# Kernel optimization log

Measured on AMD Instinct MI355X. Metric: run time of the kernel, lower is better.

## Reference

```python
import jax, jax.numpy as jnp
import numpy as np

DIM = 3072
HEADS = 24
HD = 128  # head_dim
RANK = 64
COND = 1024      # (512//8)*(512//8)*16//64
BLOCK = 2048     # main latent tokens
SEQ = BLOCK + COND
NIP = 64         # image_emb tokens
LORA_W = 1.0     # lora_weights[0]
ALPHA_SCALE = 1.0  # network_alpha / rank = 64/64
IP_SCALE = 1.0


def setup_inputs() -> dict:
    key = jax.random.key(0)
    ks = jax.random.split(key, 21)
    d = {}
    d["hidden_states"] = jax.random.normal(ks[0], (1, SEQ, DIM), jnp.float32)
    d["image_emb"] = jax.random.normal(ks[1], (1, NIP, DIM), jnp.float32)
    d["rope_cos"] = jax.random.uniform(ks[2], (SEQ, HD), jnp.float32)
    d["rope_sin"] = jax.random.uniform(ks[3], (SEQ, HD), jnp.float32)
    d["wq"] = jax.random.normal(ks[4], (DIM, DIM), jnp.float32) * 0.02
    d["bq"] = jax.random.normal(ks[5], (DIM,), jnp.float32) * 0.02
    d["wk"] = jax.random.normal(ks[6], (DIM, DIM), jnp.float32) * 0.02
    d["bk"] = jax.random.normal(ks[7], (DIM,), jnp.float32) * 0.02
    d["wv"] = jax.random.normal(ks[8], (DIM, DIM), jnp.float32) * 0.02
    d["bv"] = jax.random.normal(ks[9], (DIM,), jnp.float32) * 0.02
    d["norm_q_w"] = jax.random.uniform(ks[10], (HD,), jnp.float32, 0.5, 1.5)
    d["norm_k_w"] = jax.random.uniform(ks[11], (HD,), jnp.float32, 0.5, 1.5)
    d["q_down"] = jax.random.normal(ks[12], (RANK, DIM), jnp.float32) / RANK
    d["q_up"] = jax.random.normal(ks[13], (DIM, RANK), jnp.float32) * 0.02
    d["k_down"] = jax.random.normal(ks[14], (RANK, DIM), jnp.float32) / RANK
    d["k_up"] = jax.random.normal(ks[15], (DIM, RANK), jnp.float32) * 0.02
    d["v_down"] = jax.random.normal(ks[16], (RANK, DIM), jnp.float32) / RANK
    d["v_up"] = jax.random.normal(ks[17], (DIM, RANK), jnp.float32) * 0.02
    d["wk_ip"] = jax.random.normal(ks[18], (DIM, DIM), jnp.float32) * 0.02
    d["wv_ip"] = jax.random.normal(ks[19], (DIM, DIM), jnp.float32) * 0.02
    return d


def _rmsnorm(x, w, eps):
    v = jnp.mean(jnp.square(x), axis=-1, keepdims=True)
    y = x * jax.lax.rsqrt(v + eps)
    return y if w is None else y * w


def _heads(x, b):  # (B,S,DIM) -> (B,H,S,HD)
    return x.reshape(b, -1, HEADS, HD).transpose(0, 2, 1, 3)


def _rope(x, cos, sin):
    # diffusers apply_rotary_emb, use_real, unbind_dim=-1
    x1 = x[..., 0::2]
    x2 = x[..., 1::2]
    rot = jnp.stack([-x2, x1], axis=-1).reshape(x.shape)
    return x * cos[None, None] + rot * sin[None, None]


def _sdpa(q, k, v, bias=None):
    s = jnp.einsum("bhqd,bhkd->bhqk", q, k) / jnp.sqrt(jnp.float32(q.shape[-1]))
    if bias is not None:
        s = s + bias
    p = jax.nn.softmax(s, axis=-1)
    return jnp.einsum("bhqk,bhkd->bhqd", p, v)


def reference(hidden_states, image_emb, rope_cos, rope_sin,
              wq, bq, wk, bk, wv, bv, norm_q_w, norm_k_w,
              q_down, q_up, k_down, k_up, v_down, v_up, wk_ip, wv_ip):
    B = hidden_states.shape[0]

    # base QKV projections
    q = hidden_states @ wq.T + bq
    k = hidden_states @ wk.T + bk
    v = hidden_states @ wv.T + bv

    # original (pre-LoRA, pre-norm, pre-RoPE) query on the main block for IP attention
    original_query = _heads(hidden_states[:, :BLOCK] @ wq.T + bq, B)

    # masked LoRA add (n_loras=1): only tokens [BLOCK, BLOCK+COND) contribute
    pos = jnp.arange(SEQ)
    tok_mask = ((pos >= BLOCK) & (pos < BLOCK + COND)).astype(hidden_states.dtype)
    hm = hidden_states * tok_mask[None, :, None]
    q = q + LORA_W * ALPHA_SCALE * ((hm @ q_down.T) @ q_up.T)
    k = k + LORA_W * ALPHA_SCALE * ((hm @ k_down.T) @ k_up.T)
    v = v + LORA_W * ALPHA_SCALE * ((hm @ v_down.T) @ v_up.T)

    q = _heads(q, B)
    k = _heads(k, B)
    v = _heads(v, B)

    # per-head RMSNorm (attn.norm_q / attn.norm_k, eps=1e-6 in Flux)
    q = _rmsnorm(q, norm_q_w, 1e-6)
    k = _rmsnorm(k, norm_k_w, 1e-6)

    # IP-adapter cross attention with the original query
    ip_k = _rmsnorm(_heads(image_emb @ wk_ip.T, B), None, 1e-5)
    ip_v = _heads(image_emb @ wv_ip.T, B)
    ip_out = _sdpa(original_query, ip_k, ip_v)  # (B,H,BLOCK,HD)
    ip_out = ip_out.transpose(0, 2, 1, 3).reshape(B, -1, DIM)

    # RoPE on q/k
    q = _rope(q, rope_cos, rope_sin)
    k = _rope(k, rope_cos, rope_sin)

    # attention bias: main-block queries see everything; cond queries only their own block
    m = jnp.ones((SEQ, SEQ), jnp.float32)
    m = m.at[:BLOCK, :].set(0.0)
    m = m.at[BLOCK:BLOCK + COND, BLOCK:BLOCK + COND].set(0.0)
    bias = (m * -1e20)[None, None]

    out = _sdpa(q, k, v, bias)  # (B,H,SEQ,HD)
    out = out.transpose(0, 2, 1, 3).reshape(B, SEQ, DIM)

    main = out[:, :BLOCK, :] + IP_SCALE * ip_out
    return main
```

## Files before the change

### kernel.cpp

```cpp
#include <hip/hip_runtime.h>
#include <stdint.h>

#define DIM 3072
#define HEADS 24
#define HD 128
#define RANKN 64
#define CONDN 1024
#define BLK 2048
#define SEQN 3072
#define NIPN 64

typedef __attribute__((ext_vector_type(8))) short s8v;
typedef __attribute__((ext_vector_type(4))) float fx4;

static __device__ __forceinline__ unsigned short f2bf(float f){
  union{float f; unsigned u;} v; v.f=f;
  unsigned r = v.u + 0x7FFFu + ((v.u>>16)&1u);
  return (unsigned short)(r>>16);
}

#define GL16(g,l) __builtin_amdgcn_global_load_lds((const __attribute__((address_space(1))) void*)(g), (__attribute__((address_space(3))) void*)(l), 16, 0, 0)
#define MFMA(a,b,c) __builtin_amdgcn_mfma_f32_16x16x32_bf16((a),(b),(c),0,0,0)

__global__ __launch_bounds__(256) void cvt_f32_bf16(const float* __restrict__ src,
                                                    unsigned short* __restrict__ dst, int n4){
  int i = blockIdx.x*256 + threadIdx.x;
  if (i < n4){
    float4 v = ((const float4*)src)[i];
    ushort4 o;
    o.x = f2bf(v.x); o.y = f2bf(v.y); o.z = f2bf(v.z); o.w = f2bf(v.w);
    ((ushort4*)dst)[i] = o;
  }
}

__global__ __launch_bounds__(256) void lora_down_g(const unsigned short* __restrict__ A,
                                                   const unsigned short* __restrict__ D0,
                                                   const unsigned short* __restrict__ D1,
                                                   unsigned short* __restrict__ outb){
  __shared__ unsigned short As[128*64];
  __shared__ unsigned short Bs[64*64];
  int tid = threadIdx.x, lane = tid & 63, w = tid >> 6;
  int l15 = lane & 15, l16 = lane >> 4;
  int z = blockIdx.z;
  int m0 = blockIdx.y * 128;
  const unsigned short* Dw = z ? D1 : D0;
  int wr = w * 32;
  fx4 acc[2][4] = {};
  for (int kt = 0; kt < DIM; kt += 64){
    #pragma unroll
    for (int i = 0; i < 4; i++){
      int p = i*256 + tid;
      int row = p >> 3, cc = p & 7;
      int gc = cc ^ (row & 7);
      GL16(A + (size_t)(m0+row)*DIM + kt + gc*8, As + p*8);
    }
    #pragma unroll
    for (int i = 0; i < 2; i++){
      int p = i*256 + tid;
      int row = p >> 3, cc = p & 7;
      int gc = cc ^ (row & 7);
      GL16(Dw + (size_t)row*DIM + kt + gc*8, Bs + p*8);
    }
    __syncthreads();
    #pragma unroll
    for (int kk = 0; kk < 2; kk++){
      s8v af[2], bfr[4];
      #pragma unroll
      for (int t = 0; t < 2; t++){
        int rowa = wr + t*16 + l15;
        int ca = (kk*4 + l16) ^ (rowa & 7);
        af[t] = *(const s8v*)(As + rowa*64 + ca*8);
      }
      #pragma unroll
      for (int t = 0; t < 4; t++){
        int rowb = t*16 + l15;
        int cb = (kk*4 + l16) ^ (rowb & 7);
        bfr[t] = *(const s8v*)(Bs + rowb*64 + cb*8);
      }
      #pragma unroll
      for (int mt = 0; mt < 2; mt++)
        #pragma unroll
        for (int nt = 0; nt < 4; nt++)
          acc[mt][nt] = MFMA(af[mt], bfr[nt], acc[mt][nt]);
    }
    __syncthreads();
  }
  #pragma unroll
  for (int mt = 0; mt < 2; mt++)
    #pragma unroll
    for (int j = 0; j < 4; j++){
      int row = m0 + wr + mt*16 + l16*4 + j;
      #pragma unroll
      for (int nt = 0; nt < 4; nt++){
        int col = nt*16 + l15;
        outb[((size_t)z*CONDN + row)*64 + col] = f2bf(acc[mt][nt][j]);
      }
    }
}

#define BM 128
#define BN 128
#define BK 64
__global__ __launch_bounds__(256) void gemm_qkv2(
    const unsigned short* __restrict__ hs_bf,
    const unsigned short* __restrict__ ie_bf,
    const unsigned short* __restrict__ Wq,
    const unsigned short* __restrict__ Wk,
    const unsigned short* __restrict__ Wv,
    const unsigned short* __restrict__ Wik,
    const unsigned short* __restrict__ Wiv,
    const float* __restrict__ bq, const float* __restrict__ bk, const float* __restrict__ bv,
    const unsigned short* __restrict__ downb,
    const unsigned short* __restrict__ upk,
    const unsigned short* __restrict__ upv,
    float* __restrict__ qb, float* __restrict__ kb, float* __restrict__ vb,
    float* __restrict__ ipk_pre, float* __restrict__ ipv_pre)
{
  __shared__ unsigned short As[BM*BK];
  __shared__ unsigned short Bs[BN*BK];
  int tid = threadIdx.x, lane = tid & 63, w = tid >> 6;
  int l15 = lane & 15, l16 = lane >> 4;
  int x = blockIdx.x, y = blockIdx.y;
  int z = x / 24, n = x % 24;
  bool is_main = true;
  int z2 = 0;
  if (z == 0 && y >= 16){
    int sub = (y - 16)*24 + n;
    if (sub >= 48) return;
    is_main = false; z2 = sub / 24; n = sub % 24;
  }
  int m0 = y * 128;
  const unsigned short* A = is_main ? hs_bf : ie_bf;
  const unsigned short* B = is_main ? (z==0 ? Wq : (z==1 ? Wk : Wv))
                                    : (z2 ? Wiv : Wik);
  int n0 = n * 128;
  int wr = (w >> 1) * 64, wc = (w & 1) * 64;

  fx4 acc[4][4] = {};

  for (int kt = 0; kt < DIM; kt += BK){
    #pragma unroll
    for (int i = 0; i < 4; i++){
      int p = i*256 + tid;
      int row = p >> 3, cc = p & 7;
      int gc = cc ^ (row & 7);
      int arow = is_main ? (m0 + row) : (row > 63 ? 63 : row);
      GL16(A + (size_t)arow*DIM + kt + gc*8, As + p*8);
      GL16(B + (size_t)(n0+row)*DIM + kt + gc*8, Bs + p*8);
    }
    __syncthreads();
    #pragma unroll
    for (int kk = 0; kk < 2; kk++){
      s8v af[4], bfr[4];
      #pragma unroll
      for (int t = 0; t < 4; t++){
        int rowa = wr + t*16 + l15;
        int ca = (kk*4 + l16) ^ (rowa & 7);
        af[t] = *(const s8v*)(As + rowa*BK + ca*8);
        int rowb = wc + t*16 + l15;
        int cb = (kk*4 + l16) ^ (rowb & 7);
        bfr[t] = *(const s8v*)(Bs + rowb*BK + cb*8);
      }
      #pragma unroll
      for (int mt = 0; mt < 4; mt++)
        #pragma unroll
        for (int nt = 0; nt < 4; nt++)
          acc[mt][nt] = MFMA(af[mt], bfr[nt], acc[mt][nt]);
    }
    __syncthreads();
  }

  if (!is_main){
    float* outp = z2 ? ipv_pre : ipk_pre;
    #pragma unroll
    for (int mt = 0; mt < 4; mt++)
      #pragma unroll
      for (int j = 0; j < 4; j++){
        int row = wr + mt*16 + l16*4 + j;
        if (row < 64){
          #pragma unroll
          for (int nt = 0; nt < 4; nt++)
            outp[(size_t)row*DIM + n0 + wc + nt*16 + l15] = acc[mt][nt][j];
        }
      }
    return;
  }

  if (z >= 1 && m0 >= BLK){
    const unsigned short* dwn = downb + (size_t)(z-1)*CONDN*64 + (size_t)(m0-BLK)*64;
    const unsigned short* up  = (z==1) ? upk : upv;
    #pragma unroll
    for (int i = 0; i < 4; i++){
      int p = i*256 + tid;
      int row = p >> 3, cc = p & 7;
      int gc = cc ^ (row & 7);
      GL16(dwn + (size_t)row*64 + gc*8, As + p*8);
      GL16(up + (size_t)(n0+row)*64 + gc*8, Bs + p*8);
    }
    __syncthreads();
    #pragma unroll
    for (int kk = 0; kk < 2; kk++){
      s8v af[4], bfr[4];
      #pragma unroll
      for (int t = 0; t < 4; t++){
        int rowa = wr + t*16 + l15;
        int ca = (kk*4 + l16) ^ (rowa & 7);
        af[t] = *(const s8v*)(As + rowa*64 + ca*8);
        int rowb = wc + t*16 + l15;
        int cb = (kk*4 + l16) ^ (rowb & 7);
        bfr[t] = *(const s8v*)(Bs + rowb*64 + cb*8);
      }
      #pragma unroll
      for (int mt = 0; mt < 4; mt++)
        #pragma unroll
        for (int nt = 0; nt < 4; nt++)
          acc[mt][nt] = MFMA(af[mt], bfr[nt], acc[mt][nt]);
    }
  }

  {
    const float* bias = z==0 ? bq : (z==1 ? bk : bv);
    float* C = z==0 ? qb : (z==1 ? kb : vb);
    float bv4[4];
    #pragma unroll
    for (int nt = 0; nt < 4; nt++) bv4[nt] = bias[n0 + wc + nt*16 + l15];
    #pragma unroll
    for (int mt = 0; mt < 4; mt++)
      #pragma unroll
      for (int j = 0; j < 4; j++){
        int row = m0 + wr + mt*16 + l16*4 + j;
        float* crow = C + (size_t)row*DIM;
        #pragma unroll
        for (int nt = 0; nt < 4; nt++){
          int col = n0 + wc + nt*16 + l15;
          crow[col] = acc[mt][nt][j] + bv4[nt];
        }
      }
  }
}

__global__ __launch_bounds__(256) void norm_rope(const float* __restrict__ src,
                                                 unsigned short* __restrict__ dst,
                                                 const float* __restrict__ wt,
                                                 const float* __restrict__ rc,
                                                 const float* __restrict__ rs,
                                                 int S, float qscale){
  int tid = threadIdx.x, lane = tid & 63, w = tid >> 6;
  int r = blockIdx.x*4 + w;
  int pos = r % S, h = r / S;
  const float* x = src + (size_t)pos*DIM + h*HD;
  float2 xv = *(const float2*)(x + 2*lane);
  float ss = xv.x*xv.x + xv.y*xv.y;
  #pragma unroll
  for (int o = 1; o < 64; o <<= 1) ss += __shfl_xor(ss, o);
  float rr = rsqrtf(ss*(1.f/128.f) + 1e-6f);
  float y0 = xv.x*rr*wt[2*lane], y1 = xv.y*rr*wt[2*lane+1];
  float2 cv = *(const float2*)(rc + (size_t)pos*HD + 2*lane);
  float2 sv = *(const float2*)(rs + (size_t)pos*HD + 2*lane);
  float o0 = (y0*cv.x - y1*sv.x)*qscale;
  float o1 = (y1*cv.y + y0*sv.y)*qscale;
  ushort2 ov; ov.x = f2bf(o0); ov.y = f2bf(o1);
  *(ushort2*)(dst + ((size_t)h*S + pos)*HD + 2*lane) = ov;
}

__global__ __launch_bounds__(256) void ipk_norm_bf(const float* __restrict__ src,
                                                   unsigned short* __restrict__ dst){
  int tid = threadIdx.x, lane = tid & 63, w = tid >> 6;
  int r = blockIdx.x*4 + w;
  int pos = r / HEADS, h = r % HEADS;
  const float* x = src + (size_t)pos*DIM + h*HD;
  float2 xv = *(const float2*)(x + 2*lane);
  float ss = xv.x*xv.x + xv.y*xv.y;
  #pragma unroll
  for (int o = 1; o < 64; o <<= 1) ss += __shfl_xor(ss, o);
  float rr = rsqrtf(ss*(1.f/128.f) + 1e-5f);
  ushort2 ov; ov.x = f2bf(xv.x*rr); ov.y = f2bf(xv.y*rr);
  *(ushort2*)(dst + ((size_t)h*NIPN + pos)*HD + 2*lane) = ov;
}

__global__ __launch_bounds__(256) void ipv_transpose(const float* __restrict__ ipv,
                                                     unsigned short* __restrict__ vt){
  int h = blockIdx.x, tid = threadIdx.x;
  #pragma unroll
  for (int i = 0; i < 32; i++){
    int idx = i*256 + tid;
    int d = idx >> 6, key = idx & 63;
    vt[((size_t)h*HD + d)*64 + key] = f2bf(ipv[(size_t)key*DIM + h*HD + d]);
  }
}

__global__ __launch_bounds__(256) void v_transpose(const float* __restrict__ v,
                                                   unsigned short* __restrict__ Vt){
  __shared__ float t[64][129];
  int h = blockIdx.y, p0 = blockIdx.x*64, tid = threadIdx.x;
  int dcol = tid & 127, prow2 = tid >> 7;
  #pragma unroll
  for (int i = 0; i < 32; i++){
    int pos = i*2 + prow2;
    t[pos][dcol] = v[(size_t)(p0+pos)*DIM + h*HD + dcol];
  }
  __syncthreads();
  int pos = tid & 63, dbase = tid >> 6;
  #pragma unroll
  for (int i = 0; i < 32; i++){
    int d = i*4 + dbase;
    Vt[((size_t)h*HD + d)*SEQN + p0 + pos] = f2bf(t[pos][d]);
  }
}

__global__ __launch_bounds__(256) void ip_attn_m(const float* __restrict__ qb,
                                                 const unsigned short* __restrict__ ipk_bf,
                                                 const unsigned short* __restrict__ ipv_t,
                                                 float* __restrict__ out){
  __shared__ unsigned short Ks[64*HD];
  __shared__ unsigned short Vs[HD*64];
  __shared__ unsigned short Ps[4][16*64];
  int tid = threadIdx.x, lane = tid & 63, w = tid >> 6;
  int l15 = lane & 15, l16 = lane >> 4;
  int h = blockIdx.y;
  int q0 = blockIdx.x*64 + w*16;
  const unsigned short* Kh = ipk_bf + (size_t)h*NIPN*HD;
  const unsigned short* Vh = ipv_t + (size_t)h*HD*NIPN;

  #pragma unroll
  for (int i = 0; i < 4; i++){
    int p = i*256 + tid;
    int row = p >> 4, cc = p & 15;
    int gc = cc ^ (row & 7);
    GL16(Kh + (size_t)row*HD + gc*8, Ks + p*8);
  }
  #pragma unroll
  for (int i = 0; i < 4; i++){
    int p = i*256 + tid;
    int row = p >> 3, cc = p & 7;
    int gc = cc ^ (row & 7);
    GL16(Vh + (size_t)row*64 + gc*8, Vs + p*8);
  }

  s8v qf[4];
  #pragma unroll
  for (int kf = 0; kf < 4; kf++){
    const float* qp = qb + (size_t)(q0 + l15)*DIM + h*HD + kf*32 + l16*8;
    float4 a = *(const float4*)qp;
    float4 b = *(const float4*)(qp + 4);
    s8v f;
    f[0]=(short)f2bf(a.x); f[1]=(short)f2bf(a.y); f[2]=(short)f2bf(a.z); f[3]=(short)f2bf(a.w);
    f[4]=(short)f2bf(b.x); f[5]=(short)f2bf(b.y); f[6]=(short)f2bf(b.z); f[7]=(short)f2bf(b.w);
    qf[kf] = f;
  }
  __syncthreads();

  fx4 s[4] = {};
  #pragma unroll
  for (int ct = 0; ct < 4; ct++){
    #pragma unroll
    for (int kk = 0; kk < 4; kk++){
      int row = ct*16 + l15;
      int c = (kk*4 + l16) ^ (row & 7);
      s8v b = *(const s8v*)(Ks + row*HD + c*8);
      s[ct] = MFMA(qf[kk], b, s[ct]);
    }
  }
  const float SC = 0.08838834764831845f;
  float lrow[4];
  #pragma unroll
  for (int j = 0; j < 4; j++){
    #pragma unroll
    for (int ct = 0; ct < 4; ct++) s[ct][j] *= SC;
    float v = fmaxf(fmaxf(s[0][j], s[1][j]), fmaxf(s[2][j], s[3][j]));
    #pragma unroll
    for (int o2 = 1; o2 < 16; o2 <<= 1) v = fmaxf(v, __shfl_xor(v, o2));
    float sum = 0.f;
    #pragma unroll
    for (int ct = 0; ct < 4; ct++){
      float p = __expf(s[ct][j] - v);
      s[ct][j] = p;
      sum += p;
    }
    #pragma unroll
    for (int o2 = 1; o2 < 16; o2 <<= 1) sum += __shfl_xor(sum, o2);
    lrow[j] = sum;
  }

  #pragma unroll
  for (int ct = 0; ct < 4; ct++)
    #pragma unroll
    for (int j = 0; j < 4; j++){
      int row = l16*4 + j;
      int cidx = ct*16 + l15;
      Ps[w][row*64 + (((cidx>>3) ^ (row&7))<<3) + (cidx&7)] = f2bf(s[ct][j]);
    }
  asm volatile("s_waitcnt lgkmcnt(0)" ::: "memory");
  s8v pa[2];
  #pragma unroll
  for (int kk = 0; kk < 2; kk++){
    int c = (kk*4 + l16) ^ (l15 & 7);
    pa[kk] = *(const s8v*)(&Ps[w][l15*64 + c*8]);
  }
  fx4 o[8] = {};
  #pragma unroll
  for (int nt = 0; nt < 8; nt++){
    #pragma unroll
    for (int kk = 0; kk < 2; kk++){
      int row = nt*16 + l15;
      int c = (kk*4 + l16) ^ (row & 7);
      s8v bv = *(const s8v*)(Vs + row*64 + c*8);
      o[nt] = MFMA(pa[kk], bv, o[nt]);
    }
  }
  #pragma unroll
  for (int nt = 0; nt < 8; nt++)
    #pragma unroll
    for (int j = 0; j < 4; j++){
      int row = q0 + l16*4 + j;
      int d = nt*16 + l15;
      out[(size_t)row*DIM + h*HD + d] = o[nt][j] / lrow[j];
    }
}

#define QB 128
#define KVB 64
#define PSTR 72
__global__ __launch_bounds__(512, 4) void flash_attn_split(const unsigned short* __restrict__ Qn,
                                                           const unsigned short* __restrict__ Kn,
                                                           const unsigned short* __restrict__ Vt,
                                                           float* __restrict__ po0,
                                                           float* __restrict__ po1,
                                                           float* __restrict__ pm,
                                                           float* __restrict__ pl){
  __shared__ unsigned short Ks[KVB*HD];
  __shared__ unsigned short Vs[HD*KVB];
  __shared__ unsigned short Ps[8][16*PSTR];
  int tid = threadIdx.x, lane = tid & 63, w = tid >> 6;
  int l15 = lane & 15, l16 = lane >> 4;
  int b = blockIdx.x;
  int swz = (b & 7) * 96 + (b >> 3);
  int sp = swz / 384;
  int rem = swz - sp*384;
  int h = rem >> 4;
  int qt = rem & 15;
  int q0 = qt*QB + w*16;
  const unsigned short* Qh = Qn + (size_t)h*BLK*HD;
  const unsigned short* Kh = Kn + (size_t)h*SEQN*HD;
  const unsigned short* Vh = Vt + (size_t)h*HD*SEQN;
  const int kvbase = sp * (SEQN/2);
  const int NT = (SEQN/2) / KVB;

  s8v qf[4];
  #pragma unroll
  for (int kf = 0; kf < 4; kf++)
    qf[kf] = *(const s8v*)(Qh + (size_t)(q0 + l15)*HD + kf*32 + l16*8);

  fx4 o[8] = {};
  float mrow[4], lrow[4];
  #pragma unroll
  for (int j = 0; j < 4; j++){ mrow[j] = -1e30f; lrow[j] = 0.f; }

  for (int t = 0; t < NT; t++){
    int kv0 = kvbase + t*KVB;
    #pragma unroll
    for (int i = 0; i < 2; i++){
      int p = i*512 + tid;
      int row = p >> 4, cc = p & 15;
      int gc = cc ^ (row & 7);
      GL16(Kh + (size_t)(kv0+row)*HD + gc*8, Ks + p*8);
    }
    #pragma unroll
    for (int i = 0; i < 2; i++){
      int p = i*512 + tid;
      int row = p >> 3, cc = p & 7;
      int gc = cc ^ (row & 7);
      GL16(Vh + (size_t)row*SEQN + kv0 + gc*8, Vs + p*8);
    }
    __syncthreads();

    fx4 s[4] = {};
    #pragma unroll
    for (int ct = 0; ct < 4; ct++){
      #pragma unroll
      for (int kk = 0; kk < 4; kk++){
        int row = ct*16 + l15;
        int c = (kk*4 + l16) ^ (row & 7);
        s8v bb = *(const s8v*)(Ks + row*HD + c*8);
        s[ct] = MFMA(qf[kk], bb, s[ct]);
      }
    }
    float pmax[4], rssum[4];
    #pragma unroll
    for (int j = 0; j < 4; j++){
      float v = fmaxf(fmaxf(s[0][j], s[1][j]), fmaxf(s[2][j], s[3][j]));
      #pragma unroll
      for (int o2 = 1; o2 < 16; o2 <<= 1) v = fmaxf(v, __shfl_xor(v, o2));
      pmax[j] = v;
      rssum[j] = 0.f;
    }
    float need = 0.f;
    #pragma unroll
    for (int j = 0; j < 4; j++) need = fmaxf(need, pmax[j] - mrow[j]);
    if (__any(need > 8.f)){
      float alpha[4];
      #pragma unroll
      for (int j = 0; j < 4; j++){
        float mnew = fmaxf(mrow[j], pmax[j]);
        alpha[j] = __expf(mrow[j] - mnew);
        mrow[j] = mnew;
      }
      #pragma unroll
      for (int nt = 0; nt < 8; nt++)
        #pragma unroll
        for (int j = 0; j < 4; j++) o[nt][j] *= alpha[j];
      #pragma unroll
      for (int j = 0; j < 4; j++) lrow[j] *= alpha[j];
    }
    #pragma unroll
    for (int ct = 0; ct < 4; ct++)
      #pragma unroll
      for (int j = 0; j < 4; j++){
        float p = __expf(s[ct][j] - mrow[j]);
        s[ct][j] = p;
        rssum[j] += p;
      }
    #pragma unroll
    for (int j = 0; j < 4; j++){
      #pragma unroll
      for (int o2 = 1; o2 < 16; o2 <<= 1) rssum[j] += __shfl_xor(rssum[j], o2);
      lrow[j] += rssum[j];
    }

    #pragma unroll
    for (int ct = 0; ct < 4; ct++)
      #pragma unroll
      for (int j = 0; j < 4; j++){
        int row = l16*4 + j;
        int cidx = ct*16 + l15;
        Ps[w][row*PSTR + cidx] = f2bf(s[ct][j]);
      }
    asm volatile("s_waitcnt lgkmcnt(0)" ::: "memory");
    s8v pa[2];
    #pragma unroll
    for (int kk = 0; kk < 2; kk++)
      pa[kk] = *(const s8v*)(&Ps[w][l15*PSTR + (kk*4 + l16)*8]);
    #pragma unroll
    for (int nt = 0; nt < 8; nt++){
      #pragma unroll
      for (int kk = 0; kk < 2; kk++){
        int row = nt*16 + l15;
        int c = (kk*4 + l16) ^ (row & 7);
        s8v bvv = *(const s8v*)(Vs + row*KVB + c*8);
        o[nt] = MFMA(pa[kk], bvv, o[nt]);
      }
    }
    __syncthreads();
  }

  float* pop = sp ? po1 : po0;
  #pragma unroll
  for (int nt = 0; nt < 8; nt++)
    #pragma unroll
    for (int j = 0; j < 4; j++){
      int row = q0 + l16*4 + j;
      int d = nt*16 + l15;
      pop[((size_t)h*BLK + row)*HD + d] = o[nt][j];
    }
  if (l15 == 0){
    #pragma unroll
    for (int j = 0; j < 4; j++){
      int row = q0 + l16*4 + j;
      pm[(size_t)sp*HEADS*BLK + h*BLK + row] = mrow[j];
      pl[(size_t)sp*HEADS*BLK + h*BLK + row] = lrow[j];
    }
  }
}

__global__ __launch_bounds__(256) void flash_merge(const float* __restrict__ po0,
                                                   const float* __restrict__ po1,
                                                   const float* __restrict__ pm,
                                                   const float* __restrict__ pl,
                                                   float* __restrict__ out){
  int tid = threadIdx.x, lane = tid & 63, w = tid >> 6;
  int r = blockIdx.x*4 + w;
  int h = r >> 11, pos = r & 2047;
  float m0 = pm[r], m1 = pm[HEADS*BLK + r];
  float l0 = pl[r], l1 = pl[HEADS*BLK + r];
  float mx = fmaxf(m0, m1);
  float a0 = __expf(m0 - mx), a1 = __expf(m1 - mx);
  float li = 1.f / (l0*a0 + l1*a1);
  float s0 = a0*li, s1 = a1*li;
  size_t base = ((size_t)h*BLK + pos)*HD + 2*lane;
  float2 x0 = *(const float2*)(po0 + base);
  float2 x1 = *(const float2*)(po1 + base);
  float* op = out + (size_t)pos*DIM + h*HD + 2*lane;
  float2 cv = *(const float2*)op;
  cv.x += x0.x*s0 + x1.x*s1;
  cv.y += x0.y*s0 + x1.y*s1;
  *(float2*)op = cv;
}

extern "C" void kernel_launch(void* const* d_in, const int* in_sizes, int n_in,
                              void* d_out, int out_size, void* d_ws, size_t ws_size,
                              hipStream_t stream){
  (void)in_sizes; (void)n_in; (void)out_size;
  const float* hs       = (const float*)d_in[0];
  const float* image_emb= (const float*)d_in[1];
  const float* rope_cos = (const float*)d_in[2];
  const float* rope_sin = (const float*)d_in[3];
  const float* wq = (const float*)d_in[4];
  const float* bq = (const float*)d_in[5];
  const float* wk = (const float*)d_in[6];
  const float* bk = (const float*)d_in[7];
  const float* wv = (const float*)d_in[8];
  const float* bv = (const float*)d_in[9];
  const float* norm_q_w = (const float*)d_in[10];
  const float* norm_k_w = (const float*)d_in[11];
  const float* k_down = (const float*)d_in[14];
  const float* k_up   = (const float*)d_in[15];
  const float* v_down = (const float*)d_in[16];
  const float* v_up   = (const float*)d_in[17];
  const float* wk_ip  = (const float*)d_in[18];
  const float* wv_ip  = (const float*)d_in[19];
  float* out = (float*)d_out;

  char* ws = (char*)d_ws;
  size_t off = 0;
  auto alloc = [&](size_t bytes){ void* p = ws + off; off += (bytes + 255) & ~(size_t)255; return p; };
  unsigned short* hs_bf = (unsigned short*)alloc((size_t)SEQN*DIM*2);
  unsigned short* ie_bf = (unsigned short*)alloc((size_t)NIPN*DIM*2);
  unsigned short* w_bf[5];
  for (int i = 0; i < 5; i++) w_bf[i] = (unsigned short*)alloc((size_t)DIM*DIM*2);
  unsigned short* lw_bf[4];
  for (int i = 0; i < 4; i++) lw_bf[i] = (unsigned short*)alloc((size_t)RANKN*DIM*2);
  unsigned short* downb = (unsigned short*)alloc((size_t)2*CONDN*RANKN*2);
  float* qb = (float*)alloc((size_t)BLK*DIM*4);
  float* kb = (float*)alloc((size_t)SEQN*DIM*4);
  float* vb = (float*)alloc((size_t)SEQN*DIM*4);
  float* ipk_pre = (float*)alloc((size_t)NIPN*DIM*4);
  float* ipv_pre = (float*)alloc((size_t)NIPN*DIM*4);
  unsigned short* ipk_bf = (unsigned short*)alloc((size_t)HEADS*NIPN*HD*2);
  unsigned short* ipv_t  = (unsigned short*)alloc((size_t)HEADS*HD*NIPN*2);
  float* pm  = (float*)alloc((size_t)2*HEADS*BLK*4);
  float* pl  = (float*)alloc((size_t)2*HEADS*BLK*4);
  if (off > ws_size) return;

  unsigned short* Qn = w_bf[0];
  unsigned short* Kn = w_bf[1];
  unsigned short* Vt = w_bf[2];
  float* po0 = qb;
  float* po1 = kb;

  int n4;
  n4 = SEQN*DIM/4;
  cvt_f32_bf16<<<(n4+255)/256, 256, 0, stream>>>(hs, hs_bf, n4);
  n4 = NIPN*DIM/4;
  cvt_f32_bf16<<<(n4+255)/256, 256, 0, stream>>>(image_emb, ie_bf, n4);

  n4 = DIM*DIM/4;
  cvt_f32_bf16<<<(n4+255)/256, 256, 0, stream>>>(wq, w_bf[0], n4);
  cvt_f32_bf16<<<(n4+255)/256, 256, 0, stream>>>(wk, w_bf[1], n4);
  cvt_f32_bf16<<<(n4+255)/256, 256, 0, stream>>>(wv, w_bf[2], n4);
  cvt_f32_bf16<<<(n4+255)/256, 256, 0, stream>>>(wk_ip, w_bf[3], n4);
  cvt_f32_bf16<<<(n4+255)/256, 256, 0, stream>>>(wv_ip, w_bf[4], n4);

  n4 = RANKN*DIM/4;
  cvt_f32_bf16<<<(n4+255)/256, 256, 0, stream>>>(k_down, lw_bf[0], n4);
  cvt_f32_bf16<<<(n4+255)/256, 256, 0, stream>>>(v_down, lw_bf[1], n4);
  cvt_f32_bf16<<<(n4+255)/256, 256, 0, stream>>>(k_up,   lw_bf[2], n4);
  cvt_f32_bf16<<<(n4+255)/256, 256, 0, stream>>>(v_up,   lw_bf[3], n4);

  lora_down_g<<<dim3(1, CONDN/128, 2), 256, 0, stream>>>(hs_bf + (size_t)BLK*DIM,
      lw_bf[0], lw_bf[1], downb);

  gemm_qkv2<<<dim3(72, 24), 256, 0, stream>>>(hs_bf, ie_bf,
      w_bf[0], w_bf[1], w_bf[2], w_bf[3], w_bf[4],
      bq, bk, bv, downb, lw_bf[2], lw_bf[3],
      qb, kb, vb, ipk_pre, ipv_pre);

  ipk_norm_bf<<<(NIPN*HEADS)/4, 256, 0, stream>>>(ipk_pre, ipk_bf);
  ipv_transpose<<<HEADS, 256, 0, stream>>>(ipv_pre, ipv_t);

  const float SC = 0.08838834764831845f;
  norm_rope<<<(BLK*HEADS)/4, 256, 0, stream>>>(qb, Qn, norm_q_w, rope_cos, rope_sin, BLK, SC);
  norm_rope<<<(SEQN*HEADS)/4, 256, 0, stream>>>(kb, Kn, norm_k_w, rope_cos, rope_sin, SEQN, 1.0f);
  v_transpose<<<dim3(SEQN/64, HEADS), 256, 0, stream>>>(vb, Vt);

  ip_attn_m<<<dim3(BLK/64, HEADS), 256, 0, stream>>>(qb, ipk_bf, ipv_t, out);
  flash_attn_split<<<768, 512, 0, stream>>>(Qn, Kn, Vt, po0, po1, pm, pl);
  flash_merge<<<(HEADS*BLK)/4, 256, 0, stream>>>(po0, po1, pm, pl, out);
}
```

Baseline: 616.5 us.

## Rewrite QKV GEMM with 256x256 tiles, double-buffered LDS and XCD-aware block mapping

Replaces the 128x128 single-buffered QKV/IP projection GEMM with a 512-thread kernel that computes 256x256 output tiles. The K loop now double-buffers LDS, splitting the next-tile loads into quarter chunks that are interleaved with MFMA phases under s_setprio. A flattened 408-block grid is remapped so that consecutive tiles land on the same XCD. The goal is to raise arithmetic intensity and hide global-load latency. The cost is higher register and LDS pressure, and 408 large tiles may leave the last wave unevenly spread across CUs.

```diff
diff --git a/kernel.cpp b/kernel.cpp
--- a/kernel.cpp
+++ b/kernel.cpp
@@ -98,10 +98,7 @@
     }
 }
 
-#define BM 128
-#define BN 128
-#define BK 64
-__global__ __launch_bounds__(256) void gemm_qkv2(
+__global__ __launch_bounds__(512, 2) void gemm_256(
     const unsigned short* __restrict__ hs_bf,
     const unsigned short* __restrict__ ie_bf,
     const unsigned short* __restrict__ Wq,
@@ -116,125 +113,194 @@
     float* __restrict__ qb, float* __restrict__ kb, float* __restrict__ vb,
     float* __restrict__ ipk_pre, float* __restrict__ ipv_pre)
 {
-  __shared__ unsigned short As[BM*BK];
-  __shared__ unsigned short Bs[BN*BK];
+  __shared__ unsigned short Ab[2][16384];
+  __shared__ unsigned short Bb[2][16384];
   int tid = threadIdx.x, lane = tid & 63, w = tid >> 6;
+  int wm = w >> 2, wn = w & 3;
   int l15 = lane & 15, l16 = lane >> 4;
-  int x = blockIdx.x, y = blockIdx.y;
-  int z = x / 24, n = x % 24;
-  bool is_main = true;
-  int z2 = 0;
-  if (z == 0 && y >= 16){
-    int sub = (y - 16)*24 + n;
-    if (sub >= 48) return;
-    is_main = false; z2 = sub / 24; n = sub % 24;
-  }
-  int m0 = y * 128;
-  const unsigned short* A = is_main ? hs_bf : ie_bf;
-  const unsigned short* B = is_main ? (z==0 ? Wq : (z==1 ? Wk : Wv))
-                                    : (z2 ? Wiv : Wik);
-  int n0 = n * 128;
-  int wr = (w >> 1) * 64, wc = (w & 1) * 64;
-
-  fx4 acc[4][4] = {};
-
-  for (int kt = 0; kt < DIM; kt += BK){
+
+  int b = blockIdx.x;
+  int id = (b & 7) * 51 + (b >> 3);
+  int z, mt, ntile;
+  if (id < 96){ z = 0; mt = id / 12; ntile = id % 12; }
+  else if (id < 240){ z = 1; int r = id - 96; mt = r / 12; ntile = r % 12; }
+  else if (id < 384){ z = 2; int r = id - 240; mt = r / 12; ntile = r % 12; }
+  else { z = 3; int r = id - 384; mt = r / 12; ntile = r % 12; }
+  const bool is_ip = (z == 3);
+  int z2 = is_ip ? mt : 0;
+  int m0 = is_ip ? 0 : mt * 256;
+  int n0 = ntile * 256;
+  const unsigned short* A = is_ip ? ie_bf : hs_bf;
+  const unsigned short* B = is_ip ? (z2 ? Wiv : Wik)
+                                  : (z == 0 ? Wq : (z == 1 ? Wk : Wv));
+
+  fx4 acc[8][4] = {};
+  s8v af[8], bfr[8];
+
+  auto stA = [&](int buf, int half, int kt){
+    #pragma unroll
+    for (int i = 0; i < 2; i++){
+      int p = i*512 + tid;
+      int row = p >> 3, cc = p & 7, gc = cc ^ (row & 7);
+      int ar = m0 + half*128 + row;
+      if (is_ip && ar > 63) ar = 63;
+      GL16(A + (size_t)ar*DIM + kt + gc*8, &Ab[buf][half*8192 + p*8]);
+    }
+  };
+  auto stB = [&](int buf, int half, int kt){
+    #pragma unroll
+    for (int i = 0; i < 2; i++){
+      int p = i*512 + tid;
+      int row = p >> 3, cc = p & 7, gc = cc ^ (row & 7);
+      GL16(B + (size_t)(n0 + half*128 + row)*DIM + kt + gc*8, &Bb[buf][half*8192 + p*8]);
+    }
+  };
+  auto rdA = [&](int buf, int m, int kk)->s8v{
+    int rl = m*16 + l15;
+    return *(const s8v*)(&Ab[buf][wm*8192 + rl*64 + ((kk*4 + l16) ^ (rl & 7))*8]);
+  };
+  auto rdB = [&](int buf, int n, int kk)->s8v{
+    int rB = wn*64 + n*16 + l15;
+    return *(const s8v*)(&Bb[buf][(rB >> 7)*8192 + (rB & 127)*64 + ((kk*4 + l16) ^ (rB & 7))*8]);
+  };
+
+  stA(0,0,0); stA(0,1,0); stB(0,0,0); stB(0,1,0);
+  asm volatile("s_waitcnt vmcnt(0)" ::: "memory");
+  __builtin_amdgcn_s_barrier();
+
+  const int NT = DIM / 64;
+  for (int t = 0; t < NT; t++){
+    int cur = t & 1, nxt = cur ^ 1;
+    int kt1 = (t + 1) * 64;
+    bool pf = (t + 1 < NT);
+
+    if (pf){
+      stA(nxt, 0, kt1);
+      asm volatile("s_waitcnt vmcnt(2)" ::: "memory");
+    } else {
+      asm volatile("s_waitcnt vmcnt(0)" ::: "memory");
+    }
+    __builtin_amdgcn_s_barrier();
+    #pragma unroll
+    for (int m = 0; m < 4; m++){ af[m*2] = rdA(cur,m,0); af[m*2+1] = rdA(cur,m,1); }
+    #pragma unroll
+    for (int n = 0; n < 2; n++){ bfr[n*2] = rdB(cur,n,0); bfr[n*2+1] = rdB(cur,n,1); }
+    __builtin_amdgcn_s_setprio(1);
+    #pragma unroll
+    for (int m = 0; m < 4; m++)
+      #pragma unroll
+      for (int n = 0; n < 2; n++){
+        acc[m][n] = MFMA(af[m*2],   bfr[n*2],   acc[m][n]);
+        acc[m][n] = MFMA(af[m*2+1], bfr[n*2+1], acc[m][n]);
+      }
+    __builtin_amdgcn_s_setprio(0);
+    __builtin_amdgcn_s_barrier();
+
+    if (pf) stA(nxt, 1, kt1);
+    #pragma unroll
+    for (int n = 2; n < 4; n++){ bfr[n*2] = rdB(cur,n,0); bfr[n*2+1] = rdB(cur,n,1); }
+    __builtin_amdgcn_s_setprio(1);
+    #pragma unroll
+    for (int m = 0; m < 4; m++)
+      #pragma unroll
+      for (int n = 2; n < 4; n++){
+        acc[m][n] = MFMA(af[m*2],   bfr[n*2],   acc[m][n]);
+        acc[m][n] = MFMA(af[m*2+1], bfr[n*2+1], acc[m][n]);
+      }
+    __builtin_amdgcn_s_setprio(0);
+    __builtin_amdgcn_s_barrier();
+
+    if (pf) stB(nxt, 0, kt1);
+    #pragma unroll
+    for (int m = 4; m < 8; m++){ af[(m-4)*2] = rdA(cur,m,0); af[(m-4)*2+1] = rdA(cur,m,1); }
+    __builtin_amdgcn_s_setprio(1);
+    #pragma unroll
+    for (int m = 4; m < 8; m++)
+      #pragma unroll
+      for (int n = 2; n < 4; n++){
+        acc[m][n] = MFMA(af[(m-4)*2],   bfr[n*2],   acc[m][n]);
+        acc[m][n] = MFMA(af[(m-4)*2+1], bfr[n*2+1], acc[m][n]);
+      }
+    __builtin_amdgcn_s_setprio(0);
+    __builtin_amdgcn_s_barrier();
+
+    if (pf) stB(nxt, 1, kt1);
+    __builtin_amdgcn_s_setprio(1);
+    #pragma unroll
+    for (int m = 4; m < 8; m++)
+      #pragma unroll
+      for (int n = 0; n < 2; n++){
+        acc[m][n] = MFMA(af[(m-4)*2],   bfr[n*2],   acc[m][n]);
+        acc[m][n] = MFMA(af[(m-4)*2+1], bfr[n*2+1], acc[m][n]);
+      }
+    __builtin_amdgcn_s_setprio(0);
+    __builtin_amdgcn_s_barrier();
+  }
+
+  if (is_ip){
+    float* outp = z2 ? ipv_pre : ipk_pre;
+    if (wm == 0){
+      #pragma unroll
+      for (int m = 0; m < 4; m++)
+        #pragma unroll
+        for (int j = 0; j < 4; j++){
+          int row = m*16 + l16*4 + j;
+          #pragma unroll
+          for (int n = 0; n < 4; n++)
+            outp[(size_t)row*DIM + n0 + wn*64 + n*16 + l15] = acc[m][n][j];
+        }
+    }
+    return;
+  }
+
+  if (z >= 1 && m0 >= BLK){
+    const unsigned short* dwn = downb + (size_t)(z-1)*CONDN*64 + (size_t)(m0 - BLK)*64;
+    const unsigned short* up  = (z == 1) ? upk : upv;
     #pragma unroll
     for (int i = 0; i < 4; i++){
-      int p = i*256 + tid;
-      int row = p >> 3, cc = p & 7;
-      int gc = cc ^ (row & 7);
-      int arow = is_main ? (m0 + row) : (row > 63 ? 63 : row);
-      GL16(A + (size_t)arow*DIM + kt + gc*8, As + p*8);
-      GL16(B + (size_t)(n0+row)*DIM + kt + gc*8, Bs + p*8);
-    }
-    __syncthreads();
+      int p = i*512 + tid;
+      int row = p >> 3, cc = p & 7, gc = cc ^ (row & 7);
+      GL16(dwn + (size_t)row*64 + gc*8, &Ab[0][p*8]);
+      GL16(up + (size_t)(n0 + row)*64 + gc*8, &Bb[0][p*8]);
+    }
+    asm volatile("s_waitcnt vmcnt(0)" ::: "memory");
+    __builtin_amdgcn_s_barrier();
     #pragma unroll
     for (int kk = 0; kk < 2; kk++){
-      s8v af[4], bfr[4];
-      #pragma unroll
-      for (int t = 0; t < 4; t++){
-        int rowa = wr + t*16 + l15;
-        int ca = (kk*4 + l16) ^ (rowa & 7);
-        af[t] = *(const s8v*)(As + rowa*BK + ca*8);
-        int rowb = wc + t*16 + l15;
-        int cb = (kk*4 + l16) ^ (rowb & 7);
-        bfr[t] = *(const s8v*)(Bs + rowb*BK + cb*8);
-      }
-      #pragma unroll
-      for (int mt = 0; mt < 4; mt++)
+      s8v aL[8], bL[4];
+      #pragma unroll
+      for (int m = 0; m < 8; m++){
+        int rA = wm*128 + m*16 + l15;
+        aL[m] = *(const s8v*)(&Ab[0][rA*64 + ((kk*4 + l16) ^ (rA & 7))*8]);
+      }
+      #pragma unroll
+      for (int n = 0; n < 4; n++){
+        int rB = wn*64 + n*16 + l15;
+        bL[n] = *(const s8v*)(&Bb[0][rB*64 + ((kk*4 + l16) ^ (rB & 7))*8]);
+      }
+      #pragma unroll
+      for (int m = 0; m < 8; m++)
         #pragma unroll
-        for (int nt = 0; nt < 4; nt++)
-          acc[mt][nt] = MFMA(af[mt], bfr[nt], acc[mt][nt]);
-    }
-    __syncthreads();
-  }
-
-  if (!is_main){
-    float* outp = z2 ? ipv_pre : ipk_pre;
-    #pragma unroll
-    for (int mt = 0; mt < 4; mt++)
+        for (int n = 0; n < 4; n++)
+          acc[m][n] = MFMA(aL[m], bL[n], acc[m][n]);
+    }
+  }
+
+  {
+    const float* bias = z == 0 ? bq : (z == 1 ? bk : bv);
+    float* C = z == 0 ? qb : (z == 1 ? kb : vb);
+    float bv4[4];
+    #pragma unroll
+    for (int n = 0; n < 4; n++) bv4[n] = bias[n0 + wn*64 + n*16 + l15];
+    #pragma unroll
+    for (int m = 0; m < 8; m++)
       #pragma unroll
       for (int j = 0; j < 4; j++){
-        int row = wr + mt*16 + l16*4 + j;
-        if (row < 64){
-          #pragma unroll
-          for (int nt = 0; nt < 4; nt++)
-            outp[(size_t)row*DIM + n0 + wc + nt*16 + l15] = acc[mt][nt][j];
-        }
-      }
-    return;
-  }
-
-  if (z >= 1 && m0 >= BLK){
-    const unsigned short* dwn = downb + (size_t)(z-1)*CONDN*64 + (size_t)(m0-BLK)*64;
-    const unsigned short* up  = (z==1) ? upk : upv;
-    #pragma unroll
-    for (int i = 0; i < 4; i++){
-      int p = i*256 + tid;
-      int row = p >> 3, cc = p & 7;
-      int gc = cc ^ (row & 7);
-      GL16(dwn + (size_t)row*64 + gc*8, As + p*8);
-      GL16(up + (size_t)(n0+row)*64 + gc*8, Bs + p*8);
-    }
-    __syncthreads();
-    #pragma unroll
-    for (int kk = 0; kk < 2; kk++){
-      s8v af[4], bfr[4];
-      #pragma unroll
-      for (int t = 0; t < 4; t++){
-        int rowa = wr + t*16 + l15;
-        int ca = (kk*4 + l16) ^ (rowa & 7);
-        af[t] = *(const s8v*)(As + rowa*64 + ca*8);
-        int rowb = wc + t*16 + l15;
-        int cb = (kk*4 + l16) ^ (rowb & 7);
-        bfr[t] = *(const s8v*)(Bs + rowb*64 + cb*8);
-      }
-      #pragma unroll
-      for (int mt = 0; mt < 4; mt++)
-        #pragma unroll
-        for (int nt = 0; nt < 4; nt++)
-          acc[mt][nt] = MFMA(af[mt], bfr[nt], acc[mt][nt]);
-    }
-  }
-
-  {
-    const float* bias = z==0 ? bq : (z==1 ? bk : bv);
-    float* C = z==0 ? qb : (z==1 ? kb : vb);
-    float bv4[4];
-    #pragma unroll
-    for (int nt = 0; nt < 4; nt++) bv4[nt] = bias[n0 + wc + nt*16 + l15];
-    #pragma unroll
-    for (int mt = 0; mt < 4; mt++)
-      #pragma unroll
-      for (int j = 0; j < 4; j++){
-        int row = m0 + wr + mt*16 + l16*4 + j;
+        int row = m0 + wm*128 + m*16 + l16*4 + j;
         float* crow = C + (size_t)row*DIM;
         #pragma unroll
-        for (int nt = 0; nt < 4; nt++){
-          int col = n0 + wc + nt*16 + l15;
-          crow[col] = acc[mt][nt][j] + bv4[nt];
-        }
+        for (int n = 0; n < 4; n++)
+          crow[n0 + wn*64 + n*16 + l15] = acc[m][n][j] + bv4[n];
       }
   }
 }
@@ -669,7 +735,7 @@
   lora_down_g<<<dim3(1, CONDN/128, 2), 256, 0, stream>>>(hs_bf + (size_t)BLK*DIM,
       lw_bf[0], lw_bf[1], downb);
 
-  gemm_qkv2<<<dim3(72, 24), 256, 0, stream>>>(hs_bf, ie_bf,
+  gemm_256<<<408, 512, 0, stream>>>(hs_bf, ie_bf,
       w_bf[0], w_bf[1], w_bf[2], w_bf[3], w_bf[4],
       bq, bk, bv, downb, lw_bf[2], lw_bf[3],
       qb, kb, vb, ipk_pre, ipv_pre);
```

Result: faster. 576.6 us (-6.5%).
